# Optimization experiments

Measured on AMD Instinct MI355X. Metric: run time of the kernel, lower is better.

## Reference

```python
import jax, jax.numpy as jnp
import numpy as np

NEG_SLOPE = 0.2


def _gat_conv(x, src, dst, W, a_l, a_r, b, n_nodes, activate):
    """DGL-style GATConv. x:[N,F_in], W:[F_in,H*D], a_l/a_r/b:[H,D]."""
    H, D = a_l.shape
    feat = (x @ W).reshape(n_nodes, H, D)                      # [N,H,D]
    el = jnp.sum(feat * a_l, axis=-1)                          # [N,H]
    er = jnp.sum(feat * a_r, axis=-1)                          # [N,H]
    e = jax.nn.leaky_relu(el[src] + er[dst], NEG_SLOPE)        # [E,H]
    # edge softmax over incoming edges of each dst node (numerically stable)
    emax = jax.ops.segment_max(e, dst, num_segments=n_nodes)   # [N,H]
    emax = jnp.where(jnp.isfinite(emax), emax, 0.0)            # zero-in-degree safe
    ee = jnp.exp(e - emax[dst])                                # [E,H]
    denom = jax.ops.segment_sum(ee, dst, num_segments=n_nodes) # [N,H]
    alpha = ee / jnp.maximum(denom[dst], 1e-9)                 # [E,H]
    # aggregate alpha-weighted src features into dst
    msg = alpha[:, :, None] * feat[src]                        # [E,H,D]
    out = jax.ops.segment_sum(msg, dst, num_segments=n_nodes)  # [N,H,D]
    out = out + b
    if activate:
        out = jax.nn.elu(out)
    return out


def setup_inputs() -> dict:
    key = jax.random.key(0)
    ks = jax.random.split(key, 16)
    N, E, F_in, H, Dh, C = 50000, 800000, 256, 4, 64, 40
    s = lambda fan_in: 1.0 / np.sqrt(fan_in)
    return {
        "x": jax.random.normal(ks[0], (N, F_in), dtype=jnp.float32),
        "edge_index": jax.random.randint(ks[1], (2, E), 0, N, dtype=jnp.int32),
        "W0": jax.random.normal(ks[2], (F_in, H * Dh), dtype=jnp.float32) * s(F_in),
        "al0": jax.random.normal(ks[3], (H, Dh), dtype=jnp.float32) * s(Dh),
        "ar0": jax.random.normal(ks[4], (H, Dh), dtype=jnp.float32) * s(Dh),
        "b0": jnp.zeros((H, Dh), dtype=jnp.float32),
        "W1": jax.random.normal(ks[5], (H * Dh, H * Dh), dtype=jnp.float32) * s(H * Dh),
        "al1": jax.random.normal(ks[6], (H, Dh), dtype=jnp.float32) * s(Dh),
        "ar1": jax.random.normal(ks[7], (H, Dh), dtype=jnp.float32) * s(Dh),
        "b1": jnp.zeros((H, Dh), dtype=jnp.float32),
        "W2": jax.random.normal(ks[8], (H * Dh, H * C), dtype=jnp.float32) * s(H * Dh),
        "al2": jax.random.normal(ks[9], (H, C), dtype=jnp.float32) * s(C),
        "ar2": jax.random.normal(ks[10], (H, C), dtype=jnp.float32) * s(C),
        "b2": jnp.zeros((H, C), dtype=jnp.float32),
    }


def reference(x, edge_index, W0, al0, ar0, b0, W1, al1, ar1, b1, W2, al2, ar2, b2):
    N = x.shape[0]
    src, dst = edge_index[0], edge_index[1]
    h = _gat_conv(x, src, dst, W0, al0, ar0, b0, N, activate=True).reshape(N, -1)
    h = _gat_conv(h, src, dst, W1, al1, ar1, b1, N, activate=True).reshape(N, -1)
    out = _gat_conv(h, src, dst, W2, al2, ar2, b2, N, activate=False)
    logits = out.mean(axis=1)  # mean over heads -> [N, num_classes]
    return logits
```

## Files before the change

### kernel.cpp

```cpp
#include <hip/hip_runtime.h>
#include <hip/hip_bf16.h>
#include <math.h>

#define NEG_SLOPE 0.2f

typedef unsigned short ushortT;
typedef __attribute__((ext_vector_type(8))) short short8;
typedef __attribute__((ext_vector_type(4))) float f32x4;
typedef __attribute__((ext_vector_type(4), aligned(4))) int   int4u;

static __device__ __forceinline__ float leaky(float x){ return x > 0.f ? x : NEG_SLOPE * x; }
static __device__ __forceinline__ float elu(float x){ return x > 0.f ? x : (__expf(x) - 1.f); }

static __device__ __forceinline__ ushortT f2bf(float f){
  unsigned u = __float_as_uint(f);
  u += 0x7fff + ((u >> 16) & 1);
  return (ushortT)(u >> 16);
}
static __device__ __forceinline__ float bf2f(ushortT h){ return __uint_as_float((unsigned)h << 16); }
static __device__ __forceinline__ float bf_lo(unsigned u){ return __uint_as_float(u << 16); }
static __device__ __forceinline__ float bf_hi(unsigned u){ return __uint_as_float(u & 0xffff0000u); }


__global__ void hist_kernel(const int* __restrict__ dst, int E, int* __restrict__ counts){
  int i = blockIdx.x*blockDim.x + threadIdx.x;
  if(i < E) atomicAdd(&counts[dst[i]], 1);
}

__global__ void scan1_kernel(const int* __restrict__ counts, int N,
                             int* __restrict__ offsets, int* __restrict__ blocksums){
  __shared__ int sdata[1024];
  int i = blockIdx.x*1024 + threadIdx.x;
  int v = (i<N) ? counts[i] : 0;
  sdata[threadIdx.x] = v;
  __syncthreads();
  for(int off=1; off<1024; off<<=1){
    int t = (threadIdx.x >= off) ? sdata[threadIdx.x-off] : 0;
    __syncthreads();
    sdata[threadIdx.x] += t;
    __syncthreads();
  }
  if(i<N) offsets[i] = sdata[threadIdx.x] - v;
  if(threadIdx.x==1023) blocksums[blockIdx.x] = sdata[1023];
}

__global__ void scan2_kernel(int* __restrict__ blocksums, int nb){
  __shared__ int sdata[64];
  int v = ((int)threadIdx.x < nb) ? blocksums[threadIdx.x] : 0;
  sdata[threadIdx.x] = v;
  __syncthreads();
  for(int off=1; off<64; off<<=1){
    int t = (threadIdx.x >= off) ? sdata[threadIdx.x-off] : 0;
    __syncthreads();
    sdata[threadIdx.x] += t;
    __syncthreads();
  }
  if((int)threadIdx.x < nb) blocksums[threadIdx.x] = sdata[threadIdx.x] - v;
}

__global__ void scan3_kernel(int* __restrict__ offsets, const int* __restrict__ blocksums,
                             int N, int E, int* __restrict__ cursor){
  int i = blockIdx.x*1024 + threadIdx.x;
  if(i < N){
    int o = offsets[i] + blocksums[blockIdx.x];
    offsets[i] = o;
    cursor[i] = o;
  }
  if(i == 0) offsets[N] = E;
}

__global__ void scatter_kernel(const int* __restrict__ src, const int* __restrict__ dst, int E,
                               int* __restrict__ cursor, int* __restrict__ ssrc){
  int i = blockIdx.x*blockDim.x + threadIdx.x;
  if(i < E){
    int d = dst[i];
    int p = atomicAdd(&cursor[d], 1);
    ssrc[p] = src[i];
  }
}

__global__ __launch_bounds__(256) void wsplit_pack(const float* __restrict__ W, int N,
                              ushortT* __restrict__ Wh, ushortT* __restrict__ Wl){
  int idx = blockIdx.x*256 + threadIdx.x;
  int lane = idx & 63;
  int t  = (idx >> 6) & 7;
  int nt = idx >> 9;
  int l15 = lane & 15, quad = lane >> 4;
  int n = nt*16 + l15;
  ushortT h[8], l[8];
  #pragma unroll
  for(int j=0;j<8;j++){
    int k = t*32 + quad*8 + j;
    float v = (n < N) ? W[(size_t)k*N + n] : 0.f;
    h[j] = f2bf(v);
    l[j] = f2bf(v - bf2f(h[j]));
  }
  *(short8*)&Wh[(size_t)idx*8] = *(short8*)h;
  *(short8*)&Wl[(size_t)idx*8] = *(short8*)l;
}

__global__ __launch_bounds__(256) void xsplit_pack(const float* __restrict__ x, int M, int Mpad,
                              ushortT* __restrict__ Xh, ushortT* __restrict__ Xl){
  int idx = blockIdx.x*256 + threadIdx.x;
  if(idx >= 8*Mpad) return;
  int t = idx / Mpad, m = idx - t*Mpad;
  size_t base = (size_t)idx * 32;
  if(m < M){
    const float* xr = &x[(size_t)m*256 + t*32];
    #pragma unroll
    for(int c=0;c<4;c++){
      float4 v0 = *(const float4*)&xr[c*8];
      float4 v1 = *(const float4*)&xr[c*8+4];
      float vv[8] = {v0.x,v0.y,v0.z,v0.w,v1.x,v1.y,v1.z,v1.w};
      ushortT h[8], l[8];
      #pragma unroll
      for(int j=0;j<8;j++){
        h[j] = f2bf(vv[j]);
        l[j] = f2bf(vv[j] - bf2f(h[j]));
      }
      *(short8*)&Xh[base + c*8] = *(short8*)h;
      *(short8*)&Xl[base + c*8] = *(short8*)l;
    }
  } else {
    short8 z = {0,0,0,0,0,0,0,0};
    #pragma unroll
    for(int c=0;c<4;c++){ *(short8*)&Xh[base + c*8] = z; *(short8*)&Xl[base + c*8] = z; }
  }
}

__global__ __launch_bounds__(256) void gemm_packed(
    const ushortT* __restrict__ Ah, const ushortT* __restrict__ Al,
    const ushortT* __restrict__ Bh, const ushortT* __restrict__ Bl,
    ushortT* __restrict__ Cm, int M, int Mpad, int N, int ntiles,
    const float* __restrict__ al, const float* __restrict__ ar,
    float* __restrict__ el, float* __restrict__ er){
  const int lane = threadIdx.x & 63;
  const int wv   = threadIdx.x >> 6;
  const int l15  = lane & 15, quad = lane >> 4;
  const int m0   = blockIdx.x*32;
  const int n0   = wv*64;
  const int nt0  = n0 >> 4;

  f32x4 acc[2][4];
  #pragma unroll
  for(int i=0;i<2;i++)
    #pragma unroll
    for(int j=0;j<4;j++){ acc[i][j][0]=0.f; acc[i][j][1]=0.f; acc[i][j][2]=0.f; acc[i][j][3]=0.f; }

  #pragma unroll
  for(int t=0; t<8; t++){
    short8 a_h[2], a_l[2], b_h[4], b_l[4];
    #pragma unroll
    for(int i=0;i<2;i++){
      size_t ad = ((size_t)t*Mpad + (m0 + i*16 + l15))*32 + quad*8;
      a_h[i] = *(const short8*)&Ah[ad];
      a_l[i] = *(const short8*)&Al[ad];
    }
    #pragma unroll
    for(int j=0;j<4;j++){
      if(nt0 + j < ntiles){
        size_t bd = (((size_t)(nt0+j)*8 + t)*64 + lane)*8;
        b_h[j] = *(const short8*)&Bh[bd];
        b_l[j] = *(const short8*)&Bl[bd];
      }
    }
    #pragma unroll
    for(int i=0;i<2;i++)
      #pragma unroll
      for(int j=0;j<4;j++){
        if(nt0 + j < ntiles){
          acc[i][j] = __builtin_amdgcn_mfma_f32_16x16x32_bf16(a_h[i], b_h[j], acc[i][j], 0,0,0);
          acc[i][j] = __builtin_amdgcn_mfma_f32_16x16x32_bf16(a_h[i], b_l[j], acc[i][j], 0,0,0);
          acc[i][j] = __builtin_amdgcn_mfma_f32_16x16x32_bf16(a_l[i], b_h[j], acc[i][j], 0,0,0);
        }
      }
  }

  if(al){
    const int h = wv;
    float alv[4], arv[4];
    #pragma unroll
    for(int j=0;j<4;j++){
      alv[j] = al[h*64 + j*16 + l15];
      arv[j] = ar[h*64 + j*16 + l15];
    }
    #pragma unroll
    for(int i=0;i<2;i++){
      #pragma unroll
      for(int r=0;r<4;r++){
        float pl = acc[i][0][r]*alv[0] + acc[i][1][r]*alv[1]
                 + acc[i][2][r]*alv[2] + acc[i][3][r]*alv[3];
        float pr = acc[i][0][r]*arv[0] + acc[i][1][r]*arv[1]
                 + acc[i][2][r]*arv[2] + acc[i][3][r]*arv[3];
        #pragma unroll
        for(int off=1; off<16; off<<=1){ pl += __shfl_xor(pl,off); pr += __shfl_xor(pr,off); }
        int gm = m0 + i*16 + quad*4 + r;
        if(l15==0 && gm < M){ el[gm*4+h] = pl; er[gm*4+h] = pr; }
      }
    }
  }

  #pragma unroll
  for(int i=0;i<2;i++){
    #pragma unroll
    for(int r=0;r<4;r++){
      int gm = m0 + i*16 + quad*4 + r;
      if(gm >= M) continue;
      #pragma unroll
      for(int j=0;j<4;j++){
        int gn = n0 + j*16 + l15;
        if(gn < N) Cm[(size_t)gm*N + gn] = f2bf(acc[i][j][r]);
      }
    }
  }
}

__global__ void attn_proj_bf(const __hip_bfloat16* __restrict__ feat, const float* __restrict__ a_l,
                             const float* __restrict__ a_r, float* __restrict__ el,
                             float* __restrict__ er, int D){
  int n = blockIdx.x;
  int h = threadIdx.x >> 6;
  int lane = threadIdx.x & 63;
  float vl = 0.f, vr = 0.f;
  for(int d=lane; d<D; d+=64){
    float f = (float)feat[(size_t)n*4*D + h*D + d];
    vl = fmaf(f, a_l[h*D+d], vl);
    vr = fmaf(f, a_r[h*D+d], vr);
  }
  #pragma unroll
  for(int off=32; off; off>>=1){ vl += __shfl_down(vl,off); vr += __shfl_down(vr,off); }
  if(lane==0){ el[n*4+h] = vl; er[n*4+h] = vr; }
}

__global__ __launch_bounds__(256) void agg_kernel(const uint4* __restrict__ feat4,
                           const float* __restrict__ el, const float* __restrict__ er,
                           const int* __restrict__ offsets, const int* __restrict__ ssrc,
                           const float* __restrict__ bias,
                           ushortT* __restrict__ Hh, ushortT* __restrict__ Hl,
                           int N, int Mpad){
  int wvi  = threadIdx.x >> 6;
  int lane = threadIdx.x & 63;
  int n = blockIdx.x*4 + wvi;
  if(n >= N) return;
  const int slot = lane >> 5;
  const int wl   = lane & 31;
  const int head = wl >> 3;
  const float ern = er[n*4 + head];
  int e0 = offsets[n], e1 = offsets[n+1];
  float a0=0.f,a1=0.f,a2=0.f,a3=0.f,a4=0.f,a5=0.f,a6=0.f,a7=0.f;
  float den = 0.f;
  int e = e0;
  for(; e+7 < e1; e += 8){
    int4u sv = *(const int4u*)&ssrc[e + slot*4];
    #pragma unroll
    for(int i=0;i<4;i++){
      int s = sv[i];
      float w = __expf(leaky(el[s*4 + head] + ern));
      uint4 q = feat4[(size_t)s*32 + wl];
      a0 = fmaf(w, bf_lo(q.x), a0); a1 = fmaf(w, bf_hi(q.x), a1);
      a2 = fmaf(w, bf_lo(q.y), a2); a3 = fmaf(w, bf_hi(q.y), a3);
      a4 = fmaf(w, bf_lo(q.z), a4); a5 = fmaf(w, bf_hi(q.z), a5);
      a6 = fmaf(w, bf_lo(q.w), a6); a7 = fmaf(w, bf_hi(q.w), a7);
      den += w;
    }
  }
  for(; e < e1; e += 2){
    int ee = e + slot;
    int ec = (ee < e1) ? ee : (e1 - 1);
    int s = ssrc[ec];
    float w = (ee < e1) ? __expf(leaky(el[s*4 + head] + ern)) : 0.f;
    uint4 q = feat4[(size_t)s*32 + wl];
    a0 = fmaf(w, bf_lo(q.x), a0); a1 = fmaf(w, bf_hi(q.x), a1);
    a2 = fmaf(w, bf_lo(q.y), a2); a3 = fmaf(w, bf_hi(q.y), a3);
    a4 = fmaf(w, bf_lo(q.z), a4); a5 = fmaf(w, bf_hi(q.z), a5);
    a6 = fmaf(w, bf_lo(q.w), a6); a7 = fmaf(w, bf_hi(q.w), a7);
    den += w;
  }
  a0 += __shfl_xor(a0,32); a1 += __shfl_xor(a1,32);
  a2 += __shfl_xor(a2,32); a3 += __shfl_xor(a3,32);
  a4 += __shfl_xor(a4,32); a5 += __shfl_xor(a5,32);
  a6 += __shfl_xor(a6,32); a7 += __shfl_xor(a7,32);
  den += __shfl_xor(den,32);
  if(slot == 0){
    float inv = 1.f / fmaxf(den, 1e-9f);
    int k0 = wl*8;
    float4 b4a = *(const float4*)&bias[k0];
    float4 b4b = *(const float4*)&bias[k0+4];
    float o[8];
    o[0] = elu(a0*inv + b4a.x); o[1] = elu(a1*inv + b4a.y);
    o[2] = elu(a2*inv + b4a.z); o[3] = elu(a3*inv + b4a.w);
    o[4] = elu(a4*inv + b4b.x); o[5] = elu(a5*inv + b4b.y);
    o[6] = elu(a6*inv + b4b.z); o[7] = elu(a7*inv + b4b.w);
    ushortT hh[8], ll[8];
    #pragma unroll
    for(int j=0;j<8;j++){
      hh[j] = f2bf(o[j]);
      ll[j] = f2bf(o[j] - bf2f(hh[j]));
    }
    int t  = wl >> 2;
    int co = (wl & 3) * 8;
    size_t ad = ((size_t)t*Mpad + n)*32 + co;
    *(short8*)&Hh[ad] = *(short8*)hh;
    *(short8*)&Hl[ad] = *(short8*)ll;
  }
}

__global__ __launch_bounds__(256) void agg2_kernel(const uint4* __restrict__ feat4,
                            const float* __restrict__ el, const float* __restrict__ er,
                            const int* __restrict__ offsets, const int* __restrict__ ssrc,
                            const float* __restrict__ bias, float* __restrict__ logits,
                            int N){
  int wv = threadIdx.x >> 6;
  int lane = threadIdx.x & 63;
  int n = blockIdx.x*4 + wv;
  if(n >= N) return;
  const int slot = lane / 20;
  const int wl   = lane - slot*20;
  const int head = wl / 5;
  const float ern = er[n*4 + head];
  int e0 = offsets[n], e1 = offsets[n+1];
  float a0=0.f,a1=0.f,a2=0.f,a3=0.f,a4=0.f,a5=0.f,a6=0.f,a7=0.f;
  float den = 0.f;
  #pragma unroll 2
  for(int e = e0; e < e1; e += 3){
    int ee = e + ((slot < 3) ? slot : 2);
    int ec = (ee < e1) ? ee : (e1 - 1);
    int s = ssrc[ec];
    bool act = (slot < 3) && (ee < e1);
    float w = act ? __expf(leaky(el[s*4 + head] + ern)) : 0.f;
    uint4 q = feat4[(size_t)s*20 + wl];
    a0 = fmaf(w, bf_lo(q.x), a0); a1 = fmaf(w, bf_hi(q.x), a1);
    a2 = fmaf(w, bf_lo(q.y), a2); a3 = fmaf(w, bf_hi(q.y), a3);
    a4 = fmaf(w, bf_lo(q.z), a4); a5 = fmaf(w, bf_hi(q.z), a5);
    a6 = fmaf(w, bf_lo(q.w), a6); a7 = fmaf(w, bf_hi(q.w), a7);
    den += w;
  }
  {
    float t1, t2;
    t1 = __shfl(a0, lane+20); t2 = __shfl(a0, lane+40); a0 += t1 + t2;
    t1 = __shfl(a1, lane+20); t2 = __shfl(a1, lane+40); a1 += t1 + t2;
    t1 = __shfl(a2, lane+20); t2 = __shfl(a2, lane+40); a2 += t1 + t2;
    t1 = __shfl(a3, lane+20); t2 = __shfl(a3, lane+40); a3 += t1 + t2;
    t1 = __shfl(a4, lane+20); t2 = __shfl(a4, lane+40); a4 += t1 + t2;
    t1 = __shfl(a5, lane+20); t2 = __shfl(a5, lane+40); a5 += t1 + t2;
    t1 = __shfl(a6, lane+20); t2 = __shfl(a6, lane+40); a6 += t1 + t2;
    t1 = __shfl(a7, lane+20); t2 = __shfl(a7, lane+40); a7 += t1 + t2;
    t1 = __shfl(den, lane+20); t2 = __shfl(den, lane+40); den += t1 + t2;
  }
  if(slot == 0){
    float inv = 1.f / fmaxf(den, 1e-9f);
    float4 ba = *(const float4*)&bias[wl*8];
    float4 bb = *(const float4*)&bias[wl*8+4];
    float o[8];
    o[0] = a0*inv + ba.x; o[1] = a1*inv + ba.y; o[2] = a2*inv + ba.z; o[3] = a3*inv + ba.w;
    o[4] = a4*inv + bb.x; o[5] = a5*inv + bb.y; o[6] = a6*inv + bb.z; o[7] = a7*inv + bb.w;
    #pragma unroll
    for(int j=0;j<8;j++){
      float t = __shfl(o[j], lane+5);  o[j] += t;
      t       = __shfl(o[j], lane+10); o[j] += t;
    }
    if(wl < 5){
      float4 r0, r1;
      r0.x = 0.25f*o[0]; r0.y = 0.25f*o[1]; r0.z = 0.25f*o[2]; r0.w = 0.25f*o[3];
      r1.x = 0.25f*o[4]; r1.y = 0.25f*o[5]; r1.z = 0.25f*o[6]; r1.w = 0.25f*o[7];
      *(float4*)&logits[(size_t)n*40 + wl*8]     = r0;
      *(float4*)&logits[(size_t)n*40 + wl*8 + 4] = r1;
    }
  }
}

extern "C" void kernel_launch(void* const* d_in, const int* in_sizes, int n_in,
                              void* d_out, int out_size, void* d_ws, size_t ws_size,
                              hipStream_t stream){
  const float* x   = (const float*)d_in[0];
  const int*   eix = (const int*)  d_in[1];
  const float* W0  = (const float*)d_in[2];
  const float* al0 = (const float*)d_in[3];
  const float* ar0 = (const float*)d_in[4];
  const float* b0  = (const float*)d_in[5];
  const float* W1  = (const float*)d_in[6];
  const float* al1 = (const float*)d_in[7];
  const float* ar1 = (const float*)d_in[8];
  const float* b1  = (const float*)d_in[9];
  const float* W2  = (const float*)d_in[10];
  const float* al2 = (const float*)d_in[11];
  const float* ar2 = (const float*)d_in[12];
  const float* b2  = (const float*)d_in[13];
  float* logits = (float*)d_out;

  const int N = in_sizes[0] / 256;
  const int E = in_sizes[1] / 2;
  const int* src = eix;
  const int* dst = eix + E;
  const int nb = (N + 1023) / 1024;

  char* ws = (char*)d_ws;
  auto alloc = [&](size_t bytes)->char*{
    char* p = ws; ws += (bytes + 255) & ~(size_t)255; return p;
  };
  const int nblocksM = (N + 127)/128;
  const int Mpad = nblocksM * 128;
  const size_t apackElems = (size_t)Mpad * 256;
  int*   counts    = (int*)  alloc((size_t)N*4);
  int*   offsets   = (int*)  alloc((size_t)(N+1)*4);
  int*   cursor    = (int*)  alloc((size_t)N*4);
  int*   blocksums = (int*)  alloc((size_t)nb*4);
  int*   ssrc      = (int*)  alloc((size_t)E*4);
  __hip_bfloat16* bufF = (__hip_bfloat16*)alloc((size_t)N*256*2);
  ushortT* Hh      = (ushortT*)alloc(apackElems*2);
  ushortT* Hl      = (ushortT*)alloc(apackElems*2);
  float* el_buf    = (float*)alloc((size_t)N*4*4);
  float* er_buf    = (float*)alloc((size_t)N*4*4);
  ushortT* Wph0 = (ushortT*)alloc(16*8*64*8*2);
  ushortT* Wpl0 = (ushortT*)alloc(16*8*64*8*2);
  ushortT* Wph1 = (ushortT*)alloc(16*8*64*8*2);
  ushortT* Wpl1 = (ushortT*)alloc(16*8*64*8*2);
  ushortT* Wph2 = (ushortT*)alloc(16*8*64*8*2);
  ushortT* Wpl2 = (ushortT*)alloc(16*8*64*8*2);

  hipMemsetAsync(counts, 0, (size_t)N*4, stream);
  hist_kernel   <<<(E+255)/256, 256, 0, stream>>>(dst, E, counts);
  scan1_kernel  <<<nb, 1024, 0, stream>>>(counts, N, offsets, blocksums);
  scan2_kernel  <<<1, 64, 0, stream>>>(blocksums, nb);
  scan3_kernel  <<<nb, 1024, 0, stream>>>(offsets, blocksums, N, E, cursor);
  scatter_kernel<<<(E+255)/256, 256, 0, stream>>>(src, dst, E, cursor, ssrc);

  wsplit_pack<<<32, 256, 0, stream>>>(W0, 256, Wph0, Wpl0);
  wsplit_pack<<<32, 256, 0, stream>>>(W1, 256, Wph1, Wpl1);
  wsplit_pack<<<32, 256, 0, stream>>>(W2, 160, Wph2, Wpl2);
  int xtotal = 8 * Mpad;
  xsplit_pack<<<(xtotal+255)/256, 256, 0, stream>>>(x, N, Mpad, Hh, Hl);

  int ggBlocks = Mpad / 32;
  int aggGrid  = (N+3)/4;
  gemm_packed<<<ggBlocks, 256, 0, stream>>>(Hh, Hl, Wph0, Wpl0, (ushortT*)bufF, N, Mpad, 256, 16, al0, ar0, el_buf, er_buf);
  agg_kernel<<<aggGrid, 256, 0, stream>>>((const uint4*)bufF, el_buf, er_buf, offsets, ssrc, b0, Hh, Hl, N, Mpad);
  gemm_packed<<<ggBlocks, 256, 0, stream>>>(Hh, Hl, Wph1, Wpl1, (ushortT*)bufF, N, Mpad, 256, 16, al1, ar1, el_buf, er_buf);
  agg_kernel<<<aggGrid, 256, 0, stream>>>((const uint4*)bufF, el_buf, er_buf, offsets, ssrc, b1, Hh, Hl, N, Mpad);
  gemm_packed<<<ggBlocks, 256, 0, stream>>>(Hh, Hl, Wph2, Wpl2, (ushortT*)bufF, N, Mpad, 160, 10, nullptr, nullptr, nullptr, nullptr);
  attn_proj_bf<<<N, 256, 0, stream>>>(bufF, al2, ar2, el_buf, er_buf, 40);
  agg2_kernel<<<aggGrid, 256, 0, stream>>>((const uint4*)bufF, el_buf, er_buf, offsets, ssrc, b2, logits, N);
}
```

Baseline: 549.8 us.

## Fuse pack kernels, fold scan2 into scan3, and widen GEMM M tile

Removes the separate block-sum scan kernel by having each scan3 block serially sum preceding block sums. Merges the three weight-pack launches and the input-pack launch into a single kernel dispatched by block index. Doubles the GEMM row tile to 64 rows per block so weight fragments are reused across more rows, at the cost of more accumulator registers and fewer blocks. This requires Mpad to be a multiple of 64.

```diff
diff --git a/kernel.cpp b/kernel.cpp
--- a/kernel.cpp
+++ b/kernel.cpp
@@ -44,25 +44,18 @@
   if(threadIdx.x==1023) blocksums[blockIdx.x] = sdata[1023];
 }
 
-__global__ void scan2_kernel(int* __restrict__ blocksums, int nb){
-  __shared__ int sdata[64];
-  int v = ((int)threadIdx.x < nb) ? blocksums[threadIdx.x] : 0;
-  sdata[threadIdx.x] = v;
-  __syncthreads();
-  for(int off=1; off<64; off<<=1){
-    int t = (threadIdx.x >= off) ? sdata[threadIdx.x-off] : 0;
-    __syncthreads();
-    sdata[threadIdx.x] += t;
-    __syncthreads();
-  }
-  if((int)threadIdx.x < nb) blocksums[threadIdx.x] = sdata[threadIdx.x] - v;
-}
-
 __global__ void scan3_kernel(int* __restrict__ offsets, const int* __restrict__ blocksums,
                              int N, int E, int* __restrict__ cursor){
+  __shared__ int sbase;
+  if(threadIdx.x == 0){
+    int s = 0;
+    for(int i=0;i<(int)blockIdx.x;i++) s += blocksums[i];
+    sbase = s;
+  }
+  __syncthreads();
   int i = blockIdx.x*1024 + threadIdx.x;
   if(i < N){
-    int o = offsets[i] + blocksums[blockIdx.x];
+    int o = offsets[i] + sbase;
     offsets[i] = o;
     cursor[i] = o;
   }
@@ -79,52 +72,63 @@
   }
 }
 
-__global__ __launch_bounds__(256) void wsplit_pack(const float* __restrict__ W, int N,
-                              ushortT* __restrict__ Wh, ushortT* __restrict__ Wl){
-  int idx = blockIdx.x*256 + threadIdx.x;
-  int lane = idx & 63;
-  int t  = (idx >> 6) & 7;
-  int nt = idx >> 9;
-  int l15 = lane & 15, quad = lane >> 4;
-  int n = nt*16 + l15;
-  ushortT h[8], l[8];
-  #pragma unroll
-  for(int j=0;j<8;j++){
-    int k = t*32 + quad*8 + j;
-    float v = (n < N) ? W[(size_t)k*N + n] : 0.f;
-    h[j] = f2bf(v);
-    l[j] = f2bf(v - bf2f(h[j]));
-  }
-  *(short8*)&Wh[(size_t)idx*8] = *(short8*)h;
-  *(short8*)&Wl[(size_t)idx*8] = *(short8*)l;
-}
-
-__global__ __launch_bounds__(256) void xsplit_pack(const float* __restrict__ x, int M, int Mpad,
-                              ushortT* __restrict__ Xh, ushortT* __restrict__ Xl){
-  int idx = blockIdx.x*256 + threadIdx.x;
-  if(idx >= 8*Mpad) return;
-  int t = idx / Mpad, m = idx - t*Mpad;
-  size_t base = (size_t)idx * 32;
-  if(m < M){
-    const float* xr = &x[(size_t)m*256 + t*32];
-    #pragma unroll
-    for(int c=0;c<4;c++){
-      float4 v0 = *(const float4*)&xr[c*8];
-      float4 v1 = *(const float4*)&xr[c*8+4];
-      float vv[8] = {v0.x,v0.y,v0.z,v0.w,v1.x,v1.y,v1.z,v1.w};
-      ushortT h[8], l[8];
+__global__ __launch_bounds__(256) void pack_all(
+    const float* __restrict__ x, int M, int Mpad, int xblocks,
+    ushortT* __restrict__ Xh, ushortT* __restrict__ Xl,
+    const float* __restrict__ W0, const float* __restrict__ W1, const float* __restrict__ W2,
+    ushortT* __restrict__ Wph0, ushortT* __restrict__ Wpl0,
+    ushortT* __restrict__ Wph1, ushortT* __restrict__ Wpl1,
+    ushortT* __restrict__ Wph2, ushortT* __restrict__ Wpl2){
+  int b = blockIdx.x;
+  if(b < xblocks){
+    int idx = b*256 + threadIdx.x;
+    if(idx >= 8*Mpad) return;
+    int t = idx / Mpad, m = idx - t*Mpad;
+    size_t base = (size_t)idx * 32;
+    if(m < M){
+      const float* xr = &x[(size_t)m*256 + t*32];
       #pragma unroll
-      for(int j=0;j<8;j++){
-        h[j] = f2bf(vv[j]);
-        l[j] = f2bf(vv[j] - bf2f(h[j]));
+      for(int c=0;c<4;c++){
+        float4 v0 = *(const float4*)&xr[c*8];
+        float4 v1 = *(const float4*)&xr[c*8+4];
+        float vv[8] = {v0.x,v0.y,v0.z,v0.w,v1.x,v1.y,v1.z,v1.w};
+        ushortT h[8], l[8];
+        #pragma unroll
+        for(int j=0;j<8;j++){
+          h[j] = f2bf(vv[j]);
+          l[j] = f2bf(vv[j] - bf2f(h[j]));
+        }
+        *(short8*)&Xh[base + c*8] = *(short8*)h;
+        *(short8*)&Xl[base + c*8] = *(short8*)l;
       }
-      *(short8*)&Xh[base + c*8] = *(short8*)h;
-      *(short8*)&Xl[base + c*8] = *(short8*)l;
+    } else {
+      short8 z = {0,0,0,0,0,0,0,0};
+      #pragma unroll
+      for(int c=0;c<4;c++){ *(short8*)&Xh[base + c*8] = z; *(short8*)&Xl[base + c*8] = z; }
     }
   } else {
-    short8 z = {0,0,0,0,0,0,0,0};
-    #pragma unroll
-    for(int c=0;c<4;c++){ *(short8*)&Xh[base + c*8] = z; *(short8*)&Xl[base + c*8] = z; }
+    int wb = b - xblocks;
+    int which = wb >> 5;
+    const float* W = (which==0) ? W0 : (which==1) ? W1 : W2;
+    ushortT* Wh = (which==0) ? Wph0 : (which==1) ? Wph1 : Wph2;
+    ushortT* Wl = (which==0) ? Wpl0 : (which==1) ? Wpl1 : Wpl2;
+    int Nn = (which==2) ? 160 : 256;
+    int idx = (wb & 31)*256 + threadIdx.x;
+    int lane = idx & 63;
+    int t  = (idx >> 6) & 7;
+    int nt = idx >> 9;
+    int l15 = lane & 15, quad = lane >> 4;
+    int n = nt*16 + l15;
+    ushortT h[8], l[8];
+    #pragma unroll
+    for(int j=0;j<8;j++){
+      int k = t*32 + quad*8 + j;
+      float v = (n < Nn) ? W[(size_t)k*Nn + n] : 0.f;
+      h[j] = f2bf(v);
+      l[j] = f2bf(v - bf2f(h[j]));
+    }
+    *(short8*)&Wh[(size_t)idx*8] = *(short8*)h;
+    *(short8*)&Wl[(size_t)idx*8] = *(short8*)l;
   }
 }
 
@@ -137,21 +141,21 @@
   const int lane = threadIdx.x & 63;
   const int wv   = threadIdx.x >> 6;
   const int l15  = lane & 15, quad = lane >> 4;
-  const int m0   = blockIdx.x*32;
+  const int m0   = blockIdx.x*64;
   const int n0   = wv*64;
   const int nt0  = n0 >> 4;
 
-  f32x4 acc[2][4];
+  f32x4 acc[4][4];
   #pragma unroll
-  for(int i=0;i<2;i++)
+  for(int i=0;i<4;i++)
     #pragma unroll
     for(int j=0;j<4;j++){ acc[i][j][0]=0.f; acc[i][j][1]=0.f; acc[i][j][2]=0.f; acc[i][j][3]=0.f; }
 
   #pragma unroll
   for(int t=0; t<8; t++){
-    short8 a_h[2], a_l[2], b_h[4], b_l[4];
-    #pragma unroll
-    for(int i=0;i<2;i++){
+    short8 a_h[4], a_l[4], b_h[4], b_l[4];
+    #pragma unroll
+    for(int i=0;i<4;i++){
       size_t ad = ((size_t)t*Mpad + (m0 + i*16 + l15))*32 + quad*8;
       a_h[i] = *(const short8*)&Ah[ad];
       a_l[i] = *(const short8*)&Al[ad];
@@ -165,7 +169,7 @@
       }
     }
     #pragma unroll
-    for(int i=0;i<2;i++)
+    for(int i=0;i<4;i++)
       #pragma unroll
       for(int j=0;j<4;j++){
         if(nt0 + j < ntiles){
@@ -185,7 +189,7 @@
       arv[j] = ar[h*64 + j*16 + l15];
     }
     #pragma unroll
-    for(int i=0;i<2;i++){
+    for(int i=0;i<4;i++){
       #pragma unroll
       for(int r=0;r<4;r++){
         float pl = acc[i][0][r]*alv[0] + acc[i][1][r]*alv[1]
@@ -201,7 +205,7 @@
   }
 
   #pragma unroll
-  for(int i=0;i<2;i++){
+  for(int i=0;i<4;i++){
     #pragma unroll
     for(int r=0;r<4;r++){
       int gm = m0 + i*16 + quad*4 + r;
@@ -421,17 +425,14 @@
   hipMemsetAsync(counts, 0, (size_t)N*4, stream);
   hist_kernel   <<<(E+255)/256, 256, 0, stream>>>(dst, E, counts);
   scan1_kernel  <<<nb, 1024, 0, stream>>>(counts, N, offsets, blocksums);
-  scan2_kernel  <<<1, 64, 0, stream>>>(blocksums, nb);
   scan3_kernel  <<<nb, 1024, 0, stream>>>(offsets, blocksums, N, E, cursor);
   scatter_kernel<<<(E+255)/256, 256, 0, stream>>>(src, dst, E, cursor, ssrc);
 
-  wsplit_pack<<<32, 256, 0, stream>>>(W0, 256, Wph0, Wpl0);
-  wsplit_pack<<<32, 256, 0, stream>>>(W1, 256, Wph1, Wpl1);
-  wsplit_pack<<<32, 256, 0, stream>>>(W2, 160, Wph2, Wpl2);
-  int xtotal = 8 * Mpad;
-  xsplit_pack<<<(xtotal+255)/256, 256, 0, stream>>>(x, N, Mpad, Hh, Hl);
-
-  int ggBlocks = Mpad / 32;
+  int xblocks = (8*Mpad + 255)/256;
+  pack_all<<<xblocks + 96, 256, 0, stream>>>(x, N, Mpad, xblocks, Hh, Hl,
+                                             W0, W1, W2, Wph0, Wpl0, Wph1, Wpl1, Wph2, Wpl2);
+
+  int ggBlocks = Mpad / 64;
   int aggGrid  = (N+3)/4;
   gemm_packed<<<ggBlocks, 256, 0, stream>>>(Hh, Hl, Wph0, Wpl0, (ushortT*)bufF, N, Mpad, 256, 16, al0, ar0, el_buf, er_buf);
   agg_kernel<<<aggGrid, 256, 0, stream>>>((const uint4*)bufF, el_buf, er_buf, offsets, ssrc, b0, Hh, Hl, N, Mpad);
```

After: 553.5 us. No clear change (+0.7%).
